# Kernel tuning notes

Measured on AMD Instinct MI355X. Metric: run time of the kernel, lower is better.

The kernel has to match this reference:

```python
import jax, jax.numpy as jnp
import numpy as np

B, S, H, M = 8, 128, 768, 128
EPS = 1e-12


def setup_inputs() -> dict:
    key = jax.random.key(0)
    ks = jax.random.split(key, 8)
    seq_hiddens = jax.random.normal(ks[0], (B, S, H), dtype=jnp.float32)
    gamma = jnp.ones((H,), jnp.float32)
    beta = jnp.zeros((H,), jnp.float32)
    # conditional LN dense weights (torch Linear weight: (out, in)); small init so math stays stable
    w_beta = jax.random.normal(ks[1], (H, H), dtype=jnp.float32) * 0.02
    w_gamma = jax.random.normal(ks[2], (H, H), dtype=jnp.float32) * 0.02
    w_ent = jax.random.normal(ks[3], (H, M), dtype=jnp.float32) * 0.02
    w_head = jax.random.normal(ks[4], (H, M), dtype=jnp.float32) * 0.02
    w_tail = jax.random.normal(ks[5], (H, M), dtype=jnp.float32) * 0.02
    b_ent = jnp.zeros((M,), jnp.float32)
    b_head = jnp.zeros((M,), jnp.float32)
    b_tail = jnp.zeros((M,), jnp.float32)
    return dict(seq_hiddens=seq_hiddens, gamma=gamma, beta=beta, w_beta=w_beta,
                w_gamma=w_gamma, w_ent=w_ent, b_ent=b_ent, w_head=w_head,
                b_head=b_head, w_tail=w_tail, b_tail=b_tail)


def _handshake_cln(seq, gamma, beta, w_beta, w_gamma):
    # Triangular pair expansion in the same row-major order as the torch loop:
    # for ind in range(S): pairs (ind, ind), (ind, ind+1), ..., (ind, S-1)
    s = seq.shape[1]
    ii, jj = jnp.triu_indices(s)                 # (P,) each, P = S(S+1)/2
    x = seq[:, jj, :]                            # visible hiddens   (B, P, H)
    cond = seq[:, ii, :]                         # repeated hiddens  (B, P, H)
    beta_c = jnp.einsum('bph,oh->bpo', cond, w_beta) + beta      # (B, P, H)
    gamma_c = jnp.einsum('bph,oh->bpo', cond, w_gamma) + gamma   # (B, P, H)
    mean = jnp.mean(x, axis=-1, keepdims=True)
    out = x - mean
    var = jnp.mean(out * out, axis=-1, keepdims=True)
    std = (var + EPS) ** 2                       # NOTE: faithful to source (no sqrt)
    return out / std * gamma_c + beta_c


def reference(seq_hiddens, gamma, beta, w_beta, w_gamma, w_ent, b_ent,
              w_head, b_head, w_tail, b_tail):
    shaking = _handshake_cln(seq_hiddens, gamma, beta, w_beta, w_gamma)  # (B, P, H)
    ent = jnp.tanh(shaking @ w_ent + b_ent)      # (B, P, M)
    head = jnp.tanh(shaking @ w_head + b_head)
    tail = jnp.tanh(shaking @ w_tail + b_tail)
    return jnp.stack([ent, head, tail], axis=0)  # (3, B, P, M)
```

## Files before the change

kernel.cpp:

```cpp
#include <hip/hip_runtime.h>
#include <hip/hip_bf16.h>
#include <math.h>

#define B_   8
#define S_   128
#define H_   768
#define M_   128
#define P_   8256
#define BP_  66048
#define EPSF 1e-12f

typedef unsigned short u16;
typedef unsigned int   u32;
typedef __bf16 bfrag  __attribute__((ext_vector_type(8)));
typedef float  f32x4  __attribute__((ext_vector_type(4)));

__device__ __forceinline__ float bflo(u32 u) { return __builtin_bit_cast(float, u << 16); }
__device__ __forceinline__ float bfhi(u32 u) { return __builtin_bit_cast(float, u & 0xffff0000u); }
__device__ __forceinline__ u32 f2bf(float f) {
    u32 u = __builtin_bit_cast(u32, f);
    return (u + 0x7fffu + ((u >> 16) & 1u)) >> 16;
}
__device__ __forceinline__ u16 f2bfs(float f) { return (u16)f2bf(f); }
__device__ __forceinline__ u32 pack2(float lo, float hi) { return f2bf(lo) | (f2bf(hi) << 16); }
__device__ __forceinline__ u32 fuse2(u32 x, u32 g, u32 b) {
    float rl = fmaf(bflo(x), bflo(g), bflo(b));
    float rh = fmaf(bfhi(x), bfhi(g), bfhi(b));
    return pack2(rl, rh);
}
__device__ __forceinline__ float fast_tanh(float v) {
    float e = __expf(-2.0f * fabsf(v));
    float t = (1.0f - e) / (1.0f + e);
    return copysignf(t, v);
}

__global__ void k_convert(const float* __restrict__ wg, const float* __restrict__ wb,
                          const float* __restrict__ we, const float* __restrict__ wh,
                          const float* __restrict__ wt,
                          u16* __restrict__ wgb, u16* __restrict__ wbb, u16* __restrict__ wct)
{
    int idx = blockIdx.x * 256 + threadIdx.x;
    if (idx < 589824) {
        wgb[idx] = f2bfs(wg[idx]);
    } else if (idx < 1179648) {
        int i = idx - 589824;
        wbb[i] = f2bfs(wb[i]);
    } else {
        int i = idx - 1179648;
        int n = i / 768, h = i - n * 768;
        const float* w = (n < 128) ? we : (n < 256 ? wh : wt);
        wct[i] = f2bfs(w[h * 128 + (n & 127)]);
    }
}

__global__ void k_norm(const float* __restrict__ seq, u16* __restrict__ xn, u16* __restrict__ condb)
{
    __shared__ float red[4];
    const int row = blockIdx.x;
    const int t = threadIdx.x;
    const int lane = t & 63, wid = t >> 6;
    const float* x = seq + (size_t)row * H_;
    float x0 = x[t], x1 = x[t + 256], x2 = x[t + 512];

    float s = x0 + x1 + x2;
    for (int o = 32; o; o >>= 1) s += __shfl_xor(s, o);
    if (lane == 0) red[wid] = s;
    __syncthreads();
    float mean = (red[0] + red[1] + red[2] + red[3]) * (1.0f / 768.0f);

    float c0 = x0 - mean, c1 = x1 - mean, c2 = x2 - mean;
    float ss = c0 * c0 + c1 * c1 + c2 * c2;
    for (int o = 32; o; o >>= 1) ss += __shfl_xor(ss, o);
    __syncthreads();
    if (lane == 0) red[wid] = ss;
    __syncthreads();
    float var = (red[0] + red[1] + red[2] + red[3]) * (1.0f / 768.0f);
    float sd = var + EPSF;
    float scale = 1.0f / (sd * sd);

    u16* xr = xn + (size_t)row * H_;
    u16* cr = condb + (size_t)row * H_;
    xr[t] = f2bfs(c0 * scale); xr[t + 256] = f2bfs(c1 * scale); xr[t + 512] = f2bfs(c2 * scale);
    cr[t] = f2bfs(x0);         cr[t + 256] = f2bfs(x1);         cr[t + 512] = f2bfs(x2);
}

__global__ __launch_bounds__(256) void k_cond_gemm(
    const u16* __restrict__ Ab, const u16* __restrict__ Wg, const u16* __restrict__ Wb,
    const float* __restrict__ gamma, const float* __restrict__ beta,
    u16* __restrict__ Gc, u16* __restrict__ Bc)
{
    __shared__ u16 Ash[128 * 40];
    __shared__ u16 Bsh[128 * 40];
    const int t = threadIdx.x;
    const int row0 = blockIdx.x * 128;
    const int cb = blockIdx.y;
    const bool isg = (cb < 6);
    const int nc0 = (isg ? cb : cb - 6) * 128;
    const u16* wsrc = isg ? Wg : Wb;

    const int r = t >> 1, half = t & 1;
    const u16* ap = Ab + (size_t)(row0 + r) * H_ + half * 16;
    const u16* wp = wsrc + (size_t)(nc0 + r) * H_ + half * 16;
    u16* asto = &Ash[r * 40 + half * 16];
    u16* bsto = &Bsh[r * 40 + half * 16];

    const int lane = t & 63, wid = t >> 6;
    const int wm0 = (wid >> 1) * 64, wn0 = (wid & 1) * 64;
    const int l15 = lane & 15, quad = lane >> 4, q8 = quad * 8;

    f32x4 acc[4][4] = {};
    for (int kt = 0; kt < 24; ++kt) {
        const int k0 = kt * 32;
        uint4 a0 = *(const uint4*)(ap + k0); uint4 a1 = *(const uint4*)(ap + k0 + 8);
        uint4 w0 = *(const uint4*)(wp + k0); uint4 w1 = *(const uint4*)(wp + k0 + 8);
        *(uint4*)asto = a0; *(uint4*)(asto + 8) = a1;
        *(uint4*)bsto = w0; *(uint4*)(bsto + 8) = w1;
        __syncthreads();
        bfrag af[4], bf[4];
#pragma unroll
        for (int mi = 0; mi < 4; ++mi)
            af[mi] = *reinterpret_cast<const bfrag*>(&Ash[(wm0 + mi * 16 + l15) * 40 + q8]);
#pragma unroll
        for (int ni = 0; ni < 4; ++ni)
            bf[ni] = *reinterpret_cast<const bfrag*>(&Bsh[(wn0 + ni * 16 + l15) * 40 + q8]);
#pragma unroll
        for (int mi = 0; mi < 4; ++mi)
#pragma unroll
            for (int ni = 0; ni < 4; ++ni)
                acc[mi][ni] = __builtin_amdgcn_mfma_f32_16x16x32_bf16(af[mi], bf[ni], acc[mi][ni], 0, 0, 0);
        __syncthreads();
    }

    const float* bias = isg ? gamma : beta;
    u16* outp = isg ? Gc : Bc;
#pragma unroll
    for (int mi = 0; mi < 4; ++mi)
#pragma unroll
        for (int ni = 0; ni < 4; ++ni) {
            int c = wn0 + ni * 16 + l15;
            float bv = bias[nc0 + c];
#pragma unroll
            for (int reg = 0; reg < 4; ++reg) {
                int rg = wm0 + mi * 16 + quad * 4 + reg;
                outp[(size_t)(row0 + rg) * H_ + nc0 + c] = f2bfs(acc[mi][ni][reg] + bv);
            }
        }
}

__global__ __launch_bounds__(256) void k_pair_gemm(
    const u16* __restrict__ Xn, const u16* __restrict__ Gcb, const u16* __restrict__ Bcb,
    const u16* __restrict__ WcT,
    const float* __restrict__ b_ent, const float* __restrict__ b_head, const float* __restrict__ b_tail,
    float* __restrict__ out)
{
    __shared__ u16 Ash[128 * 40];
    __shared__ u16 Bsh[128 * 40];
    __shared__ int offx[128];
    __shared__ int offc[128];

    const int t = threadIdx.x;
    const int row0 = blockIdx.x * 128;
    const int cb = blockIdx.y;

    if (t < 128) {
        int gp = row0 + t;
        int b = gp / P_;
        int p = gp - b * P_;
        int i = (int)((257.0f - sqrtf(66049.0f - 8.0f * (float)p)) * 0.5f);
        if (i < 0) i = 0; if (i > 127) i = 127;
        while (i > 0 && (i * (257 - i)) / 2 > p) --i;
        while (((i + 1) * (256 - i)) / 2 <= p) ++i;
        int j = i + (p - (i * (257 - i)) / 2);
        offx[t] = b * 128 + j;
        offc[t] = b * 128 + i;
    }
    __syncthreads();

    const int r = t >> 1, half = t & 1;
    const u16* xp = Xn + (size_t)offx[r] * H_ + half * 16;
    const u16* gp_ = Gcb + (size_t)offc[r] * H_ + half * 16;
    const u16* bp_ = Bcb + (size_t)offc[r] * H_ + half * 16;
    const u16* wp = WcT + (size_t)(cb * 128 + r) * H_ + half * 16;
    u16* asto = &Ash[r * 40 + half * 16];
    u16* bsto = &Bsh[r * 40 + half * 16];

    const int lane = t & 63, wid = t >> 6;
    const int wm0 = (wid >> 1) * 64, wn0 = (wid & 1) * 64;
    const int l15 = lane & 15, quad = lane >> 4, q8 = quad * 8;

    f32x4 acc[4][4] = {};
    for (int kt = 0; kt < 24; ++kt) {
        const int k0 = kt * 32;
        uint4 xv0 = *(const uint4*)(xp + k0);  uint4 xv1 = *(const uint4*)(xp + k0 + 8);
        uint4 gv0 = *(const uint4*)(gp_ + k0); uint4 gv1 = *(const uint4*)(gp_ + k0 + 8);
        uint4 bv0 = *(const uint4*)(bp_ + k0); uint4 bv1 = *(const uint4*)(bp_ + k0 + 8);
        uint4 wv0 = *(const uint4*)(wp + k0);  uint4 wv1 = *(const uint4*)(wp + k0 + 8);
        uint4 av0, av1;
        av0.x = fuse2(xv0.x, gv0.x, bv0.x); av0.y = fuse2(xv0.y, gv0.y, bv0.y);
        av0.z = fuse2(xv0.z, gv0.z, bv0.z); av0.w = fuse2(xv0.w, gv0.w, bv0.w);
        av1.x = fuse2(xv1.x, gv1.x, bv1.x); av1.y = fuse2(xv1.y, gv1.y, bv1.y);
        av1.z = fuse2(xv1.z, gv1.z, bv1.z); av1.w = fuse2(xv1.w, gv1.w, bv1.w);
        *(uint4*)asto = av0; *(uint4*)(asto + 8) = av1;
        *(uint4*)bsto = wv0; *(uint4*)(bsto + 8) = wv1;
        __syncthreads();
        bfrag af[4], bf[4];
#pragma unroll
        for (int mi = 0; mi < 4; ++mi)
            af[mi] = *reinterpret_cast<const bfrag*>(&Ash[(wm0 + mi * 16 + l15) * 40 + q8]);
#pragma unroll
        for (int ni = 0; ni < 4; ++ni)
            bf[ni] = *reinterpret_cast<const bfrag*>(&Bsh[(wn0 + ni * 16 + l15) * 40 + q8]);
#pragma unroll
        for (int mi = 0; mi < 4; ++mi)
#pragma unroll
            for (int ni = 0; ni < 4; ++ni)
                acc[mi][ni] = __builtin_amdgcn_mfma_f32_16x16x32_bf16(af[mi], bf[ni], acc[mi][ni], 0, 0, 0);
        __syncthreads();
    }

    const float* bias = (cb == 0) ? b_ent : (cb == 1 ? b_head : b_tail);
#pragma unroll
    for (int mi = 0; mi < 4; ++mi)
#pragma unroll
        for (int ni = 0; ni < 4; ++ni) {
            int c = wn0 + ni * 16 + l15;
            float bv = bias[c];
#pragma unroll
            for (int reg = 0; reg < 4; ++reg) {
                int rg = wm0 + mi * 16 + quad * 4 + reg;
                size_t gp2 = (size_t)row0 + rg;
                out[((size_t)cb * BP_ + gp2) * M_ + c] = fast_tanh(acc[mi][ni][reg] + bv);
            }
        }
}

extern "C" void kernel_launch(void* const* d_in, const int* in_sizes, int n_in,
                              void* d_out, int out_size, void* d_ws, size_t ws_size,
                              hipStream_t stream)
{
    const float* seq     = (const float*)d_in[0];
    const float* gamma   = (const float*)d_in[1];
    const float* beta    = (const float*)d_in[2];
    const float* w_beta  = (const float*)d_in[3];
    const float* w_gamma = (const float*)d_in[4];
    const float* w_ent   = (const float*)d_in[5];
    const float* b_ent   = (const float*)d_in[6];
    const float* w_head  = (const float*)d_in[7];
    const float* b_head  = (const float*)d_in[8];
    const float* w_tail  = (const float*)d_in[9];
    const float* b_tail  = (const float*)d_in[10];
    float* out = (float*)d_out;

    char* ws = (char*)d_ws;
    u16* xn    = (u16*)ws; ws += (size_t)1024 * 768 * 2;
    u16* condb = (u16*)ws; ws += (size_t)1024 * 768 * 2;
    u16* wgb   = (u16*)ws; ws += (size_t)768 * 768 * 2;
    u16* wbb   = (u16*)ws; ws += (size_t)768 * 768 * 2;
    u16* wct   = (u16*)ws; ws += (size_t)384 * 768 * 2;
    u16* gc    = (u16*)ws; ws += (size_t)1024 * 768 * 2;
    u16* bc    = (u16*)ws; ws += (size_t)1024 * 768 * 2;

    hipLaunchKernelGGL(k_convert, dim3(5760), dim3(256), 0, stream,
                       w_gamma, w_beta, w_ent, w_head, w_tail, wgb, wbb, wct);
    hipLaunchKernelGGL(k_norm, dim3(1024), dim3(256), 0, stream, seq, xn, condb);
    hipLaunchKernelGGL(k_cond_gemm, dim3(8, 12), dim3(256), 0, stream,
                       condb, wgb, wbb, gamma, beta, gc, bc);
    hipLaunchKernelGGL(k_pair_gemm, dim3(516, 3), dim3(256), 0, stream,
                       xn, gc, bc, wct, b_ent, b_head, b_tail, out);
}
```

Baseline: 246.6 us.

## Switch to fp16 with packed FMA and widen pair-GEMM N tile to 192

All intermediate buffers and MFMAs move from bf16 to fp16. This lets the conditional-LN fuse (x*gamma_c+beta_c) use packed __hfma2 instead of unpack, fp32 FMA and manual rounding. The pair GEMM now covers 192 output columns per block over 2 column blocks instead of 3, so the gathered A-operand fuse and its loads run twice per row tile rather than three times. It also uses a 64-wide K tile with biases merged into one buffer. The cond GEMM is retiled to 64x64 blocks for more parallelism. fp16 has less range than bf16, which could overflow if the normalised values are large, and the larger accumulator tile raises register pressure.

New measurement: 265.3 us. 1.08x slower.

```diff
diff --git a/kernel.cpp b/kernel.cpp
--- a/kernel.cpp
+++ b/kernel.cpp
@@ -1,5 +1,6 @@
 #include <hip/hip_runtime.h>
 #include <hip/hip_bf16.h>
+#include <hip/hip_fp16.h>
 #include <math.h>
 
 #define B_   8
@@ -12,21 +13,15 @@
 
 typedef unsigned short u16;
 typedef unsigned int   u32;
-typedef __bf16 bfrag  __attribute__((ext_vector_type(8)));
-typedef float  f32x4  __attribute__((ext_vector_type(4)));
-
-__device__ __forceinline__ float bflo(u32 u) { return __builtin_bit_cast(float, u << 16); }
-__device__ __forceinline__ float bfhi(u32 u) { return __builtin_bit_cast(float, u & 0xffff0000u); }
-__device__ __forceinline__ u32 f2bf(float f) {
-    u32 u = __builtin_bit_cast(u32, f);
-    return (u + 0x7fffu + ((u >> 16) & 1u)) >> 16;
-}
-__device__ __forceinline__ u16 f2bfs(float f) { return (u16)f2bf(f); }
-__device__ __forceinline__ u32 pack2(float lo, float hi) { return f2bf(lo) | (f2bf(hi) << 16); }
+typedef _Float16 h16;
+typedef _Float16 ffrag __attribute__((ext_vector_type(8)));
+typedef float    f32x4 __attribute__((ext_vector_type(4)));
+
 __device__ __forceinline__ u32 fuse2(u32 x, u32 g, u32 b) {
-    float rl = fmaf(bflo(x), bflo(g), bflo(b));
-    float rh = fmaf(bfhi(x), bfhi(g), bfhi(b));
-    return pack2(rl, rh);
+    __half2 r = __hfma2(__builtin_bit_cast(__half2, x),
+                        __builtin_bit_cast(__half2, g),
+                        __builtin_bit_cast(__half2, b));
+    return __builtin_bit_cast(u32, r);
 }
 __device__ __forceinline__ float fast_tanh(float v) {
     float e = __expf(-2.0f * fabsf(v));
@@ -37,23 +32,29 @@
 __global__ void k_convert(const float* __restrict__ wg, const float* __restrict__ wb,
                           const float* __restrict__ we, const float* __restrict__ wh,
                           const float* __restrict__ wt,
-                          u16* __restrict__ wgb, u16* __restrict__ wbb, u16* __restrict__ wct)
+                          const float* __restrict__ be, const float* __restrict__ bh,
+                          const float* __restrict__ bt,
+                          h16* __restrict__ wgb, h16* __restrict__ wbb,
+                          h16* __restrict__ wct, float* __restrict__ biasc)
 {
     int idx = blockIdx.x * 256 + threadIdx.x;
     if (idx < 589824) {
-        wgb[idx] = f2bfs(wg[idx]);
+        wgb[idx] = (h16)wg[idx];
     } else if (idx < 1179648) {
         int i = idx - 589824;
-        wbb[i] = f2bfs(wb[i]);
-    } else {
+        wbb[i] = (h16)wb[i];
+    } else if (idx < 1474560) {
         int i = idx - 1179648;
         int n = i / 768, h = i - n * 768;
         const float* w = (n < 128) ? we : (n < 256 ? wh : wt);
-        wct[i] = f2bfs(w[h * 128 + (n & 127)]);
-    }
-}
-
-__global__ void k_norm(const float* __restrict__ seq, u16* __restrict__ xn, u16* __restrict__ condb)
+        wct[i] = (h16)w[h * 128 + (n & 127)];
+    } else if (idx < 1474944) {
+        int n = idx - 1474560;
+        biasc[n] = (n < 128) ? be[n] : (n < 256 ? bh[n - 128] : bt[n - 256]);
+    }
+}
+
+__global__ void k_norm(const float* __restrict__ seq, h16* __restrict__ xn, h16* __restrict__ condb)
 {
     __shared__ float red[4];
     const int row = blockIdx.x;
@@ -78,89 +79,91 @@
     float sd = var + EPSF;
     float scale = 1.0f / (sd * sd);
 
-    u16* xr = xn + (size_t)row * H_;
-    u16* cr = condb + (size_t)row * H_;
-    xr[t] = f2bfs(c0 * scale); xr[t + 256] = f2bfs(c1 * scale); xr[t + 512] = f2bfs(c2 * scale);
-    cr[t] = f2bfs(x0);         cr[t + 256] = f2bfs(x1);         cr[t + 512] = f2bfs(x2);
+    h16* xr = xn + (size_t)row * H_;
+    h16* cr = condb + (size_t)row * H_;
+    xr[t] = (h16)(c0 * scale); xr[t + 256] = (h16)(c1 * scale); xr[t + 512] = (h16)(c2 * scale);
+    cr[t] = (h16)x0;           cr[t + 256] = (h16)x1;           cr[t + 512] = (h16)x2;
 }
 
 __global__ __launch_bounds__(256) void k_cond_gemm(
-    const u16* __restrict__ Ab, const u16* __restrict__ Wg, const u16* __restrict__ Wb,
+    const h16* __restrict__ Ab, const h16* __restrict__ Wg, const h16* __restrict__ Wb,
     const float* __restrict__ gamma, const float* __restrict__ beta,
-    u16* __restrict__ Gc, u16* __restrict__ Bc)
-{
-    __shared__ u16 Ash[128 * 40];
-    __shared__ u16 Bsh[128 * 40];
+    h16* __restrict__ Gc, h16* __restrict__ Bc)
+{
+    __shared__ h16 Ash[64 * 72];
+    __shared__ h16 Bsh[64 * 72];
     const int t = threadIdx.x;
-    const int row0 = blockIdx.x * 128;
-    const int cb = blockIdx.y;
-    const bool isg = (cb < 6);
-    const int nc0 = (isg ? cb : cb - 6) * 128;
-    const u16* wsrc = isg ? Wg : Wb;
-
-    const int r = t >> 1, half = t & 1;
-    const u16* ap = Ab + (size_t)(row0 + r) * H_ + half * 16;
-    const u16* wp = wsrc + (size_t)(nc0 + r) * H_ + half * 16;
-    u16* asto = &Ash[r * 40 + half * 16];
-    u16* bsto = &Bsh[r * 40 + half * 16];
+    const int row0 = blockIdx.x * 64;
+    const int by = blockIdx.y;
+    const bool isg = (by < 12);
+    const int nc0 = (isg ? by : by - 12) * 64;
+    const h16* wsrc = isg ? Wg : Wb;
+
+    const int r = t >> 2, q = t & 3;
+    const h16* ap = Ab + (size_t)(row0 + r) * H_ + q * 16;
+    const h16* wp = wsrc + (size_t)(nc0 + r) * H_ + q * 16;
+    h16* asto = &Ash[r * 72 + q * 16];
+    h16* bsto = &Bsh[r * 72 + q * 16];
 
     const int lane = t & 63, wid = t >> 6;
-    const int wm0 = (wid >> 1) * 64, wn0 = (wid & 1) * 64;
+    const int wm0 = (wid >> 1) * 32, wn0 = (wid & 1) * 32;
     const int l15 = lane & 15, quad = lane >> 4, q8 = quad * 8;
 
-    f32x4 acc[4][4] = {};
-    for (int kt = 0; kt < 24; ++kt) {
-        const int k0 = kt * 32;
+    f32x4 acc[2][2] = {};
+    for (int kt = 0; kt < 12; ++kt) {
+        const int k0 = kt * 64;
         uint4 a0 = *(const uint4*)(ap + k0); uint4 a1 = *(const uint4*)(ap + k0 + 8);
         uint4 w0 = *(const uint4*)(wp + k0); uint4 w1 = *(const uint4*)(wp + k0 + 8);
         *(uint4*)asto = a0; *(uint4*)(asto + 8) = a1;
         *(uint4*)bsto = w0; *(uint4*)(bsto + 8) = w1;
         __syncthreads();
-        bfrag af[4], bf[4];
-#pragma unroll
-        for (int mi = 0; mi < 4; ++mi)
-            af[mi] = *reinterpret_cast<const bfrag*>(&Ash[(wm0 + mi * 16 + l15) * 40 + q8]);
-#pragma unroll
-        for (int ni = 0; ni < 4; ++ni)
-            bf[ni] = *reinterpret_cast<const bfrag*>(&Bsh[(wn0 + ni * 16 + l15) * 40 + q8]);
-#pragma unroll
-        for (int mi = 0; mi < 4; ++mi)
-#pragma unroll
-            for (int ni = 0; ni < 4; ++ni)
-                acc[mi][ni] = __builtin_amdgcn_mfma_f32_16x16x32_bf16(af[mi], bf[ni], acc[mi][ni], 0, 0, 0);
+#pragma unroll
+        for (int ks = 0; ks < 64; ks += 32) {
+            ffrag af[2], bf[2];
+#pragma unroll
+            for (int mi = 0; mi < 2; ++mi)
+                af[mi] = *reinterpret_cast<const ffrag*>(&Ash[(wm0 + mi * 16 + l15) * 72 + ks + q8]);
+#pragma unroll
+            for (int ni = 0; ni < 2; ++ni)
+                bf[ni] = *reinterpret_cast<const ffrag*>(&Bsh[(wn0 + ni * 16 + l15) * 72 + ks + q8]);
+#pragma unroll
+            for (int mi = 0; mi < 2; ++mi)
+#pragma unroll
+                for (int ni = 0; ni < 2; ++ni)
+                    acc[mi][ni] = __builtin_amdgcn_mfma_f32_16x16x32_f16(af[mi], bf[ni], acc[mi][ni], 0, 0, 0);
+        }
         __syncthreads();
     }
 
     const float* bias = isg ? gamma : beta;
-    u16* outp = isg ? Gc : Bc;
-#pragma unroll
-    for (int mi = 0; mi < 4; ++mi)
-#pragma unroll
-        for (int ni = 0; ni < 4; ++ni) {
+    h16* outp = isg ? Gc : Bc;
+#pragma unroll
+    for (int mi = 0; mi < 2; ++mi)
+#pragma unroll
+        for (int ni = 0; ni < 2; ++ni) {
             int c = wn0 + ni * 16 + l15;
             float bv = bias[nc0 + c];
 #pragma unroll
             for (int reg = 0; reg < 4; ++reg) {
                 int rg = wm0 + mi * 16 + quad * 4 + reg;
-                outp[(size_t)(row0 + rg) * H_ + nc0 + c] = f2bfs(acc[mi][ni][reg] + bv);
+                outp[(size_t)(row0 + rg) * H_ + nc0 + c] = (h16)(acc[mi][ni][reg] + bv);
             }
         }
 }
 
 __global__ __launch_bounds__(256) void k_pair_gemm(
-    const u16* __restrict__ Xn, const u16* __restrict__ Gcb, const u16* __restrict__ Bcb,
-    const u16* __restrict__ WcT,
-    const float* __restrict__ b_ent, const float* __restrict__ b_head, const float* __restrict__ b_tail,
+    const h16* __restrict__ Xn, const h16* __restrict__ Gcb, const h16* __restrict__ Bcb,
+    const h16* __restrict__ WcT, const float* __restrict__ biasc,
     float* __restrict__ out)
 {
-    __shared__ u16 Ash[128 * 40];
-    __shared__ u16 Bsh[128 * 40];
+    __shared__ h16 Ash[128 * 72];
+    __shared__ h16 Bsh[192 * 72];
     __shared__ int offx[128];
     __shared__ int offc[128];
 
     const int t = threadIdx.x;
     const int row0 = blockIdx.x * 128;
-    const int cb = blockIdx.y;
+    const int nb = blockIdx.y;
 
     if (t < 128) {
         int gp = row0 + t;
@@ -177,59 +180,80 @@
     __syncthreads();
 
     const int r = t >> 1, half = t & 1;
-    const u16* xp = Xn + (size_t)offx[r] * H_ + half * 16;
-    const u16* gp_ = Gcb + (size_t)offc[r] * H_ + half * 16;
-    const u16* bp_ = Bcb + (size_t)offc[r] * H_ + half * 16;
-    const u16* wp = WcT + (size_t)(cb * 128 + r) * H_ + half * 16;
-    u16* asto = &Ash[r * 40 + half * 16];
-    u16* bsto = &Bsh[r * 40 + half * 16];
+    const h16* xp  = Xn  + (size_t)offx[r] * H_ + half * 32;
+    const h16* gp_ = Gcb + (size_t)offc[r] * H_ + half * 32;
+    const h16* bp_ = Bcb + (size_t)offc[r] * H_ + half * 32;
+    h16* asto = &Ash[r * 72 + half * 32];
+    const h16* wbase = WcT + (size_t)nb * 192 * H_;
 
     const int lane = t & 63, wid = t >> 6;
-    const int wm0 = (wid >> 1) * 64, wn0 = (wid & 1) * 64;
+    const int wm0 = (wid >> 1) * 64, wn0 = (wid & 1) * 96;
     const int l15 = lane & 15, quad = lane >> 4, q8 = quad * 8;
 
-    f32x4 acc[4][4] = {};
-    for (int kt = 0; kt < 24; ++kt) {
-        const int k0 = kt * 32;
-        uint4 xv0 = *(const uint4*)(xp + k0);  uint4 xv1 = *(const uint4*)(xp + k0 + 8);
-        uint4 gv0 = *(const uint4*)(gp_ + k0); uint4 gv1 = *(const uint4*)(gp_ + k0 + 8);
-        uint4 bv0 = *(const uint4*)(bp_ + k0); uint4 bv1 = *(const uint4*)(bp_ + k0 + 8);
-        uint4 wv0 = *(const uint4*)(wp + k0);  uint4 wv1 = *(const uint4*)(wp + k0 + 8);
-        uint4 av0, av1;
-        av0.x = fuse2(xv0.x, gv0.x, bv0.x); av0.y = fuse2(xv0.y, gv0.y, bv0.y);
-        av0.z = fuse2(xv0.z, gv0.z, bv0.z); av0.w = fuse2(xv0.w, gv0.w, bv0.w);
-        av1.x = fuse2(xv1.x, gv1.x, bv1.x); av1.y = fuse2(xv1.y, gv1.y, bv1.y);
-        av1.z = fuse2(xv1.z, gv1.z, bv1.z); av1.w = fuse2(xv1.w, gv1.w, bv1.w);
-        *(uint4*)asto = av0; *(uint4*)(asto + 8) = av1;
-        *(uint4*)bsto = wv0; *(uint4*)(bsto + 8) = wv1;
-        __syncthreads();
-        bfrag af[4], bf[4];
-#pragma unroll
-        for (int mi = 0; mi < 4; ++mi)
-            af[mi] = *reinterpret_cast<const bfrag*>(&Ash[(wm0 + mi * 16 + l15) * 40 + q8]);
-#pragma unroll
-        for (int ni = 0; ni < 4; ++ni)
-            bf[ni] = *reinterpret_cast<const bfrag*>(&Bsh[(wn0 + ni * 16 + l15) * 40 + q8]);
-#pragma unroll
-        for (int mi = 0; mi < 4; ++mi)
-#pragma unroll
-            for (int ni = 0; ni < 4; ++ni)
-                acc[mi][ni] = __builtin_amdgcn_mfma_f32_16x16x32_bf16(af[mi], bf[ni], acc[mi][ni], 0, 0, 0);
-        __syncthreads();
-    }
-
-    const float* bias = (cb == 0) ? b_ent : (cb == 1 ? b_head : b_tail);
+    f32x4 acc[4][6] = {};
+    for (int kt = 0; kt < 12; ++kt) {
+        const int k0 = kt * 64;
+        uint4 xv0 = *(const uint4*)(xp + k0);       uint4 xv1 = *(const uint4*)(xp + k0 + 8);
+        uint4 xv2 = *(const uint4*)(xp + k0 + 16);  uint4 xv3 = *(const uint4*)(xp + k0 + 24);
+        uint4 gv0 = *(const uint4*)(gp_ + k0);      uint4 gv1 = *(const uint4*)(gp_ + k0 + 8);
+        uint4 gv2 = *(const uint4*)(gp_ + k0 + 16); uint4 gv3 = *(const uint4*)(gp_ + k0 + 24);
+        uint4 bv0 = *(const uint4*)(bp_ + k0);      uint4 bv1 = *(const uint4*)(bp_ + k0 + 8);
+        uint4 bv2 = *(const uint4*)(bp_ + k0 + 16); uint4 bv3 = *(const uint4*)(bp_ + k0 + 24);
+        uint4 wv[6];
+#pragma unroll
+        for (int i6 = 0; i6 < 6; ++i6) {
+            int g = t + 256 * i6;
+            int brow = g >> 3, kc = g & 7;
+            wv[i6] = *(const uint4*)(wbase + (size_t)brow * H_ + k0 + kc * 8);
+        }
+        uint4 a0, a1, a2, a3;
+        a0.x = fuse2(xv0.x, gv0.x, bv0.x); a0.y = fuse2(xv0.y, gv0.y, bv0.y);
+        a0.z = fuse2(xv0.z, gv0.z, bv0.z); a0.w = fuse2(xv0.w, gv0.w, bv0.w);
+        a1.x = fuse2(xv1.x, gv1.x, bv1.x); a1.y = fuse2(xv1.y, gv1.y, bv1.y);
+        a1.z = fuse2(xv1.z, gv1.z, bv1.z); a1.w = fuse2(xv1.w, gv1.w, bv1.w);
+        a2.x = fuse2(xv2.x, gv2.x, bv2.x); a2.y = fuse2(xv2.y, gv2.y, bv2.y);
+        a2.z = fuse2(xv2.z, gv2.z, bv2.z); a2.w = fuse2(xv2.w, gv2.w, bv2.w);
+        a3.x = fuse2(xv3.x, gv3.x, bv3.x); a3.y = fuse2(xv3.y, gv3.y, bv3.y);
+        a3.z = fuse2(xv3.z, gv3.z, bv3.z); a3.w = fuse2(xv3.w, gv3.w, bv3.w);
+        *(uint4*)asto = a0; *(uint4*)(asto + 8) = a1;
+        *(uint4*)(asto + 16) = a2; *(uint4*)(asto + 24) = a3;
+#pragma unroll
+        for (int i6 = 0; i6 < 6; ++i6) {
+            int g = t + 256 * i6;
+            int brow = g >> 3, kc = g & 7;
+            *(uint4*)&Bsh[brow * 72 + kc * 8] = wv[i6];
+        }
+        __syncthreads();
+#pragma unroll
+        for (int ks = 0; ks < 64; ks += 32) {
+            ffrag af[4], bf[6];
+#pragma unroll
+            for (int mi = 0; mi < 4; ++mi)
+                af[mi] = *reinterpret_cast<const ffrag*>(&Ash[(wm0 + mi * 16 + l15) * 72 + ks + q8]);
+#pragma unroll
+            for (int ni = 0; ni < 6; ++ni)
+                bf[ni] = *reinterpret_cast<const ffrag*>(&Bsh[(wn0 + ni * 16 + l15) * 72 + ks + q8]);
+#pragma unroll
+            for (int mi = 0; mi < 4; ++mi)
+#pragma unroll
+                for (int ni = 0; ni < 6; ++ni)
+                    acc[mi][ni] = __builtin_amdgcn_mfma_f32_16x16x32_f16(af[mi], bf[ni], acc[mi][ni], 0, 0, 0);
+        }
+        __syncthreads();
+    }
+
 #pragma unroll
     for (int mi = 0; mi < 4; ++mi)
 #pragma unroll
-        for (int ni = 0; ni < 4; ++ni) {
-            int c = wn0 + ni * 16 + l15;
-            float bv = bias[c];
+        for (int ni = 0; ni < 6; ++ni) {
+            int cg = nb * 192 + wn0 + ni * 16 + l15;
+            int head = cg >> 7, m = cg & 127;
+            float bv = biasc[cg];
 #pragma unroll
             for (int reg = 0; reg < 4; ++reg) {
                 int rg = wm0 + mi * 16 + quad * 4 + reg;
                 size_t gp2 = (size_t)row0 + rg;
-                out[((size_t)cb * BP_ + gp2) * M_ + c] = fast_tanh(acc[mi][ni][reg] + bv);
+                out[((size_t)head * BP_ + gp2) * M_ + m] = fast_tanh(acc[mi][ni][reg] + bv);
             }
         }
 }
@@ -252,19 +276,21 @@
     float* out = (float*)d_out;
 
     char* ws = (char*)d_ws;
-    u16* xn    = (u16*)ws; ws += (size_t)1024 * 768 * 2;
-    u16* condb = (u16*)ws; ws += (size_t)1024 * 768 * 2;
-    u16* wgb   = (u16*)ws; ws += (size_t)768 * 768 * 2;
-    u16* wbb   = (u16*)ws; ws += (size_t)768 * 768 * 2;
-    u16* wct   = (u16*)ws; ws += (size_t)384 * 768 * 2;
-    u16* gc    = (u16*)ws; ws += (size_t)1024 * 768 * 2;
-    u16* bc    = (u16*)ws; ws += (size_t)1024 * 768 * 2;
-
-    hipLaunchKernelGGL(k_convert, dim3(5760), dim3(256), 0, stream,
-                       w_gamma, w_beta, w_ent, w_head, w_tail, wgb, wbb, wct);
+    h16* xn    = (h16*)ws; ws += (size_t)1024 * 768 * 2;
+    h16* condb = (h16*)ws; ws += (size_t)1024 * 768 * 2;
+    h16* wgb   = (h16*)ws; ws += (size_t)768 * 768 * 2;
+    h16* wbb   = (h16*)ws; ws += (size_t)768 * 768 * 2;
+    h16* wct   = (h16*)ws; ws += (size_t)384 * 768 * 2;
+    h16* gc    = (h16*)ws; ws += (size_t)1024 * 768 * 2;
+    h16* bc    = (h16*)ws; ws += (size_t)1024 * 768 * 2;
+    float* biasc = (float*)ws; ws += 384 * 4;
+
+    hipLaunchKernelGGL(k_convert, dim3(5763), dim3(256), 0, stream,
+                       w_gamma, w_beta, w_ent, w_head, w_tail, b_ent, b_head, b_tail,
+                       wgb, wbb, wct, biasc);
     hipLaunchKernelGGL(k_norm, dim3(1024), dim3(256), 0, stream, seq, xn, condb);
-    hipLaunchKernelGGL(k_cond_gemm, dim3(8, 12), dim3(256), 0, stream,
+    hipLaunchKernelGGL(k_cond_gemm, dim3(16, 24), dim3(256), 0, stream,
                        condb, wgb, wbb, gamma, beta, gc, bc);
-    hipLaunchKernelGGL(k_pair_gemm, dim3(516, 3), dim3(256), 0, stream,
-                       xn, gc, bc, wct, b_ent, b_head, b_tail, out);
-}
+    hipLaunchKernelGGL(k_pair_gemm, dim3(516, 2), dim3(256), 0, stream,
+                       xn, gc, bc, wct, biasc, out);
+}
```
